# Kernel optimization log

Hardware: AMD Instinct MI355X
Metric: run time of the kernel (lower is better)

The kernel has to match this reference:

```python
import jax, jax.numpy as jnp
import numpy as np

B, T, W = 64, 64, 20
VIDEO_DIM = 1024
JOINT_DIM = 1024
K, STRIDE = 4, 4
MARGIN = 0.2
EPS = 1e-8


def _l2norm(x, axis=-1):
    n = jnp.sqrt(jnp.sum(x * x, axis=axis, keepdims=True))
    return x / jnp.maximum(n, EPS)


def _conv1d(x, w, b, stride):
    # x: (B, C, L), w: (O, I, K) -> (B, O, L_out), VALID padding (padding=0)
    y = jax.lax.conv_general_dilated(x, w, (stride,), 'VALID',
                                     dimension_numbers=('NCH', 'OIH', 'NCH'))
    return y + b[None, :, None]


def _diag_loss(scores, margin):
    # faithful port of diag(): row/column margin costs with zeroed diagonal
    b = scores.shape[0]
    d = jnp.diagonal(scores)
    off = 1.0 - jnp.eye(b, dtype=scores.dtype)
    cost_s = jnp.maximum(margin + scores - d[:, None], 0.0) * off
    cost_im = jnp.maximum(margin + scores - d[None, :], 0.0) * off
    return cost_s.sum() / b + cost_im.sum() / b


def setup_inputs() -> dict:
    key = jax.random.key(0)
    ks = jax.random.split(key, 10)
    def g(k, shape, scale=0.02):
        return jax.random.normal(k, shape, dtype=jnp.float32) * scale
    return dict(
        video=jax.random.normal(ks[0], (B, T, VIDEO_DIM), dtype=jnp.float32),
        words=jax.random.normal(ks[1], (B, W, JOINT_DIM), dtype=jnp.float32),
        w_masks=jnp.ones((B, W), dtype=jnp.int32),
        sentences=jax.random.normal(ks[2], (B, JOINT_DIM), dtype=jnp.float32),
        conv0_w=g(ks[3], (JOINT_DIM, VIDEO_DIM, K)),
        conv0_b=jnp.zeros((JOINT_DIM,), jnp.float32),
        conv1_w=g(ks[4], (JOINT_DIM, JOINT_DIM, K)),
        conv1_b=jnp.zeros((JOINT_DIM,), jnp.float32),
        conv2_w=g(ks[5], (JOINT_DIM, JOINT_DIM, K)),
        conv2_b=jnp.zeros((JOINT_DIM,), jnp.float32),
        conv1d_w=g(ks[6], (JOINT_DIM, JOINT_DIM, 1)),
        conv1d_b=jnp.zeros((JOINT_DIM,), jnp.float32),
        fc_w=g(ks[7], (JOINT_DIM, JOINT_DIM)),
        fc_b=jnp.zeros((JOINT_DIM,), jnp.float32),
    )


def reference(video, words, w_masks, sentences,
              conv0_w, conv0_b, conv1_w, conv1_b, conv2_w, conv2_b,
              conv1d_w, conv1d_b, fc_w, fc_b):
    # Vectorizes the original per-sample python loop over the pair axes (i=sentence, j=video).
    x = jnp.transpose(video, (0, 2, 1))          # (B, C, T)
    wmask = (w_masks > 0)                        # (B, W)
    conv_params = [(conv0_w, conv0_b), (conv1_w, conv1_b), (conv2_w, conv2_b)]
    sims = []
    v_tmp = x
    for cw, cb in conv_params:
        v_tmp = jax.nn.relu(_conv1d(v_tmp, cw, cb, STRIDE))
        v = jnp.transpose(_conv1d(v_tmp, conv1d_w, conv1d_b, 1), (0, 2, 1))  # (B, Tl, D)
        # frame_by_word: masked softmax attention of frames over words
        att = jnp.einsum('jtd,iwd->ijtw', v, words)            # (i, j, Tl, W)
        att = jnp.where(wmask[:, None, None, :], att, -1e30)
        att = jax.nn.softmax(att, axis=-1)
        v_s = jnp.einsum('ijtw,iwd->ijtd', att, words)         # attended word ctx
        # cosine sim of l2-normed vectors == dot product
        sim = jnp.einsum('jtd,ijtd->ijt', _l2norm(v), _l2norm(v_s))
        sims.append(sim)
    score_all = jnp.concatenate(sims, axis=2)    # (B, B, T_total=21)
    # torch code sorts descending then means over dim 1 -> mean is sort-invariant
    scores = score_all.mean(axis=2)              # (B, B) local scores
    positive_map = score_all[jnp.arange(B), jnp.arange(B)]     # (B, T_total)
    # global branch: final conv output has length 1 -> squeeze
    g_v = _l2norm(v_tmp[:, :, 0] @ fc_w.T + fc_b)              # (B, D), unit norm
    g_scores = _l2norm(sentences) @ g_v.T                      # [i, j] = cos(g_v[j], sent[i])
    loss = _diag_loss(scores, MARGIN) + _diag_loss(g_scores, MARGIN)
    return loss, positive_map
```

## Files before the change

kernel.cpp:

```cpp
#include <hip/hip_runtime.h>
#include <cmath>
#include <cstdint>


typedef __bf16 bf16_t;
typedef bf16_t bf16x8 __attribute__((ext_vector_type(8)));
typedef bf16_t bf16x4 __attribute__((ext_vector_type(4)));
typedef float  f32x4  __attribute__((ext_vector_type(4)));

__device__ __forceinline__ void gload_lds16(const void* g, void* l) {
    __builtin_amdgcn_global_load_lds(
        (const __attribute__((address_space(1))) void*)g,
        (__attribute__((address_space(3))) void*)l, 16, 0, 0);
}

__device__ __forceinline__ int swz(int r, int c) { return (r * 8 + (c ^ (r & 7))) * 8; }

__device__ __forceinline__ int remap1(int gm) {
    if (gm < 1024) return (gm >> 4) * 21 + (gm & 15);
    if (gm < 1280) { int g = gm - 1024; return (g >> 2) * 21 + 16 + (g & 3); }
    return (gm - 1280) * 21 + 20;
}

__global__ void prep_kernel(
    const float* __restrict__ c0w, const float* __restrict__ c1w,
    const float* __restrict__ c2w,
    bf16_t* __restrict__ WT0, bf16_t* __restrict__ WT1, bf16_t* __restrict__ WT2,
    const float* __restrict__ video, bf16_t* __restrict__ Vb,
    const float* __restrict__ words, bf16_t* __restrict__ Wordsb,
    const float* __restrict__ c1dw, bf16_t* __restrict__ C1b,
    const float* __restrict__ fcw, bf16_t* __restrict__ Fb)
{
    int bx = blockIdx.x;
    if (bx < 12288) {
        const float* w; bf16_t* wt;
        if (bx < 4096)      { w = c0w; wt = WT0; }
        else if (bx < 8192) { w = c1w; wt = WT1; bx -= 4096; }
        else                { w = c2w; wt = WT2; bx -= 8192; }
        int idx = bx * 256 + threadIdx.x;
        int i = idx & 1023, o = idx >> 10;
        float4 v = *(const float4*)(w + ((size_t)o << 12) + (i << 2));
        bf16_t* base = wt + ((size_t)o << 12) + i;
        base[0]    = (bf16_t)v.x;
        base[1024] = (bf16_t)v.y;
        base[2048] = (bf16_t)v.z;
        base[3072] = (bf16_t)v.w;
    } else {
        const float* s; bf16_t* d;
        if (bx < 16384)      { s = video; d = Vb;     bx -= 12288; }
        else if (bx < 17664) { s = words; d = Wordsb; bx -= 16384; }
        else if (bx < 18688) { s = c1dw;  d = C1b;    bx -= 17664; }
        else                 { s = fcw;   d = Fb;     bx -= 18688; }
        int off = (bx * 256 + threadIdx.x) * 4;
        float4 v = *(const float4*)(s + off);
        bf16x4 o4 = { (bf16_t)v.x, (bf16_t)v.y, (bf16_t)v.z, (bf16_t)v.w };
        *(bf16x4*)(d + off) = o4;
    }
}

__global__ __launch_bounds__(256) void mgemm_kernel(
    const bf16_t* __restrict__ A, const bf16_t* __restrict__ B,
    const bf16_t* __restrict__ B2, float* __restrict__ CP,
    int N, int K, int Kchunk, int fcTile, int aRow0, int cpSlice)
{
    __shared__ __align__(16) bf16_t sA[2][4096];
    __shared__ __align__(16) bf16_t sB[2][4096];
    const int tid  = threadIdx.x;
    const int lane = tid & 63;
    const int wave = tid >> 6;
    const int bx = blockIdx.x;
    const int m0C = bx * 64;
    int m0A = m0C;
    const bf16_t* Buse = B;
    if (bx == fcTile) { m0A = aRow0; Buse = B2; }
    const int n0 = blockIdx.y * 64;
    const int k0 = blockIdx.z * Kchunk;

    const int sr = tid >> 3;
    const int pc = tid & 7;
    const int lc = pc ^ (sr & 7);
    const bf16_t* Ag = A + (size_t)(m0A + sr) * K + lc * 8;
    const bf16_t* Bg = Buse + (size_t)(n0 + sr) * K + lc * 8;
    const size_t rowskip = (size_t)32 * K;

    const int wr = (wave >> 1) * 32;
    const int wc = (wave & 1) * 32;
    const int fm = lane & 15;
    const int cb = lane >> 4;

    int offA[2][2], offB[2][2];
    #pragma unroll
    for (int h = 0; h < 2; h++) {
        offA[h][0] = swz(wr +      fm, cb + h * 4);
        offA[h][1] = swz(wr + 16 + fm, cb + h * 4);
        offB[h][0] = swz(wc +      fm, cb + h * 4);
        offB[h][1] = swz(wc + 16 + fm, cb + h * 4);
    }

    f32x4 acc[2][2];
    #pragma unroll
    for (int a = 0; a < 2; a++)
        #pragma unroll
        for (int b = 0; b < 2; b++) acc[a][b] = (f32x4){0.f, 0.f, 0.f, 0.f};

    const int nIt = Kchunk >> 6;
    {
        const bf16_t* a = Ag + k0; const bf16_t* b = Bg + k0;
        gload_lds16(a,           &sA[0][tid * 8]);
        gload_lds16(a + rowskip, &sA[0][2048 + tid * 8]);
        gload_lds16(b,           &sB[0][tid * 8]);
        gload_lds16(b + rowskip, &sB[0][2048 + tid * 8]);
    }
    for (int it = 0; it < nIt; ++it) {
        const int buf = it & 1;
        __syncthreads();
        if (it + 1 < nIt) {
            const bf16_t* a = Ag + k0 + (it + 1) * 64;
            const bf16_t* b = Bg + k0 + (it + 1) * 64;
            bf16_t* dA = &sA[buf ^ 1][0];
            bf16_t* dB = &sB[buf ^ 1][0];
            gload_lds16(a,           dA + tid * 8);
            gload_lds16(a + rowskip, dA + 2048 + tid * 8);
            gload_lds16(b,           dB + tid * 8);
            gload_lds16(b + rowskip, dB + 2048 + tid * 8);
        }
        #pragma unroll
        for (int h = 0; h < 2; h++) {
            bf16x8 a0 = *(const bf16x8*)&sA[buf][offA[h][0]];
            bf16x8 a1 = *(const bf16x8*)&sA[buf][offA[h][1]];
            bf16x8 b0 = *(const bf16x8*)&sB[buf][offB[h][0]];
            bf16x8 b1 = *(const bf16x8*)&sB[buf][offB[h][1]];
            acc[0][0] = __builtin_amdgcn_mfma_f32_16x16x32_bf16(a0, b0, acc[0][0], 0, 0, 0);
            acc[0][1] = __builtin_amdgcn_mfma_f32_16x16x32_bf16(a0, b1, acc[0][1], 0, 0, 0);
            acc[1][0] = __builtin_amdgcn_mfma_f32_16x16x32_bf16(a1, b0, acc[1][0], 0, 0, 0);
            acc[1][1] = __builtin_amdgcn_mfma_f32_16x16x32_bf16(a1, b1, acc[1][1], 0, 0, 0);
        }
    }

    float* Cz = CP + (size_t)blockIdx.z * cpSlice;
    #pragma unroll
    for (int im = 0; im < 2; im++)
        #pragma unroll
        for (int rr = 0; rr < 4; rr++) {
            int gm = m0C + wr + im * 16 + (lane >> 4) * 4 + rr;
            #pragma unroll
            for (int in_ = 0; in_ < 2; in_++) {
                int cg = n0 + wc + in_ * 16 + (lane & 15);
                Cz[(size_t)gm * N + cg] = acc[im][in_][rr];
            }
        }
}

__global__ void epilogueB_kernel(const float* __restrict__ CP_, int nz,
    const float* __restrict__ bias, bf16_t* __restrict__ D, int MN, int N, int relu)
{
    int idx = blockIdx.x * 256 + threadIdx.x;
    if (idx >= MN) return;
    int n = idx % N;
    float s = 0.f;
    for (int z = 0; z < nz; z++) s += CP_[(size_t)z * MN + idx];
    if (bias) s += bias[n];
    if (relu) s = fmaxf(s, 0.f);
    D[idx] = (bf16_t)s;
}

__global__ void epilogueCF_kernel(const float* __restrict__ CP_,
    const float* __restrict__ bias1, const float* __restrict__ biasf,
    bf16_t* __restrict__ VCb, float* __restrict__ GV)
{
    int idx = blockIdx.x * 256 + threadIdx.x;
    int row = idx >> 10, n = idx & 1023;
    float s = CP_[idx] + CP_[idx + 1441792] + CP_[idx + 2 * 1441792] + CP_[idx + 3 * 1441792];
    if (row < 1344) VCb[(size_t)remap1(row) * 1024 + n] = (bf16_t)(s + bias1[n]);
    else            GV[(size_t)(row - 1344) * 1024 + n] = s + biasf[n];
}

__global__ void normgram_kernel(const bf16_t* __restrict__ VCb, float* __restrict__ VN,
                                const bf16_t* __restrict__ Wb, float* __restrict__ G)
{
    int bx = blockIdx.x;
    if (bx < 1344) {
        const bf16_t* x = VCb + ((size_t)bx << 10);
        float s = 0.f;
        for (int d = threadIdx.x; d < 1024; d += 256) { float v = (float)x[d]; s += v * v; }
        #pragma unroll
        for (int o = 32; o; o >>= 1) s += __shfl_xor(s, o, 64);
        __shared__ float red[4];
        if ((threadIdx.x & 63) == 0) red[threadIdx.x >> 6] = s;
        __syncthreads();
        if (threadIdx.x == 0) VN[bx] = sqrtf(red[0] + red[1] + red[2] + red[3]);
    } else {
        int g = bx - 1344;
        int i = g / 100, piece = g % 100;
        int wave = threadIdx.x >> 6, lane = threadIdx.x & 63;
        int pair = piece * 4 + wave;
        int w = pair / 20, w2 = pair % 20;
        const bf16_t* a = Wb + (((size_t)i * 20 + w)  << 10) + lane * 16;
        const bf16_t* b = Wb + (((size_t)i * 20 + w2) << 10) + lane * 16;
        bf16x8 a0 = *(const bf16x8*)a, a1 = *(const bf16x8*)(a + 8);
        bf16x8 b0 = *(const bf16x8*)b, b1 = *(const bf16x8*)(b + 8);
        float s = 0.f;
        #pragma unroll
        for (int e = 0; e < 8; e++)
            s += (float)a0[e] * (float)b0[e] + (float)a1[e] * (float)b1[e];
        #pragma unroll
        for (int o = 32; o; o >>= 1) s += __shfl_xor(s, o, 64);
        if (lane == 0) G[(size_t)i * 400 + pair] = s;
    }
}

__global__ __launch_bounds__(256) void sim_kernel(
    const float* __restrict__ CPat, const float* __restrict__ G_,
    const float* __restrict__ VN_, const int* __restrict__ wmask,
    float* __restrict__ SA_)
{
    __shared__ float Gs[400];
    __shared__ float msk[20];
    const int i  = blockIdx.x;
    const int jt = blockIdx.y * 256 + threadIdx.x;
    for (int q = threadIdx.x; q < 400; q += 256) Gs[q] = G_[(size_t)i * 400 + q];
    if (threadIdx.x < 20) msk[threadIdx.x] = (wmask[i * 20 + threadIdx.x] != 0) ? 1.f : 0.f;
    __syncthreads();
    if (jt >= 1344) return;

    float s[20], p[20];
    float mx = -1e30f;
    #pragma unroll
    for (int w = 0; w < 20; w++) {
        size_t q = (size_t)(i * 20 + w) * 1344 + jt;
        s[w] = CPat[q] + CPat[q + 1720320];
        if (msk[w] != 0.f) mx = fmaxf(mx, s[w]);
    }
    float denom = 0.f, num = 0.f;
    #pragma unroll
    for (int w = 0; w < 20; w++) {
        p[w] = (msk[w] != 0.f) ? __expf(s[w] - mx) : 0.f;
        denom += p[w];
        num   += p[w] * s[w];
    }
    float quad = 0.f;
    #pragma unroll
    for (int w = 0; w < 20; w++) {
        float c = 0.f;
        #pragma unroll
        for (int w2 = 0; w2 < 20; w2++) c += Gs[w * 20 + w2] * p[w2];
        quad += p[w] * c;
    }
    float dot = num / denom;
    float vsn = sqrtf(fmaxf(quad, 0.f)) / denom;
    float sim = dot / (fmaxf(VN_[jt], 1e-8f) * fmaxf(vsn, 1e-8f));
    SA_[(size_t)i * 1344 + jt] = sim;
}

__global__ void scores_l2_kernel(const float* __restrict__ SA_, float* __restrict__ SC_,
                                 float* __restrict__ out,
                                 const float* __restrict__ GV, float* __restrict__ GN,
                                 const float* __restrict__ sent, float* __restrict__ SN)
{
    int bx = blockIdx.x;
    if (bx < 16) {
        int idx = bx * 256 + threadIdx.x;
        int i = idx >> 6, j = idx & 63;
        const float* row = SA_ + (size_t)idx * 21;
        float s = 0.f;
        #pragma unroll
        for (int t = 0; t < 21; t++) s += row[t];
        SC_[idx] = s * (1.0f / 21.0f);
        if (i == j) {
            #pragma unroll
            for (int t = 0; t < 21; t++) out[1 + i * 21 + t] = row[t];
        }
    } else {
        int b2 = bx - 16;
        int r = b2 & 63;
        const float* x = (b2 < 64 ? GV : sent) + ((size_t)r << 10);
        float*       y = (b2 < 64 ? GN : SN)   + ((size_t)r << 10);
        float s = 0.f;
        for (int d = threadIdx.x; d < 1024; d += 256) { float v = x[d]; s += v * v; }
        #pragma unroll
        for (int o = 32; o; o >>= 1) s += __shfl_xor(s, o, 64);
        __shared__ float red[4];
        __shared__ float tot;
        if ((threadIdx.x & 63) == 0) red[threadIdx.x >> 6] = s;
        __syncthreads();
        if (threadIdx.x == 0) tot = 1.0f / fmaxf(sqrtf(red[0] + red[1] + red[2] + red[3]), 1e-8f);
        __syncthreads();
        float inv = tot;
        for (int d = threadIdx.x; d < 1024; d += 256) y[d] = x[d] * inv;
    }
}

__global__ void gscore_kernel(const float* __restrict__ SN_, const float* __restrict__ GN_,
                              float* __restrict__ GS_) {
    int item = blockIdx.x * 4 + (threadIdx.x >> 6);
    int i = item >> 6, j = item & 63;
    int lane = threadIdx.x & 63;
    const float* a = SN_ + (size_t)i * 1024;
    const float* b = GN_ + (size_t)j * 1024;
    float s = 0.f;
    #pragma unroll
    for (int q = 0; q < 16; q++) { int d = lane + 64 * q; s += a[d] * b[d]; }
    #pragma unroll
    for (int o = 32; o; o >>= 1) s += __shfl_xor(s, o, 64);
    if (lane == 0) GS_[item] = s;
}

__global__ void loss_kernel(const float* __restrict__ SC_, const float* __restrict__ GS_,
                            float* __restrict__ out) {
    __shared__ float d1[64], d2[64], red[4];
    int tid = threadIdx.x;
    if (tid < 64) { d1[tid] = SC_[tid * 65]; d2[tid] = GS_[tid * 65]; }
    __syncthreads();
    float acc = 0.f;
    for (int idx = tid; idx < 4096; idx += 256) {
        int i = idx >> 6, j = idx & 63;
        if (i != j) {
            float s = SC_[idx];
            acc += fmaxf(0.2f + s - d1[i], 0.f) + fmaxf(0.2f + s - d1[j], 0.f);
            float g = GS_[idx];
            acc += fmaxf(0.2f + g - d2[i], 0.f) + fmaxf(0.2f + g - d2[j], 0.f);
        }
    }
    #pragma unroll
    for (int o = 32; o; o >>= 1) acc += __shfl_xor(acc, o, 64);
    if ((tid & 63) == 0) red[tid >> 6] = acc;
    __syncthreads();
    if (tid == 0) out[0] = (red[0] + red[1] + red[2] + red[3]) * (1.0f / 64.0f);
}

extern "C" void kernel_launch(void* const* d_in, const int* in_sizes, int n_in,
                              void* d_out, int out_size, void* d_ws, size_t ws_size,
                              hipStream_t stream)
{
    const float* video     = (const float*)d_in[0];
    const float* words     = (const float*)d_in[1];
    const int*   w_masks   = (const int*)  d_in[2];
    const float* sentences = (const float*)d_in[3];
    const float* conv0_w   = (const float*)d_in[4];
    const float* conv0_b   = (const float*)d_in[5];
    const float* conv1_w   = (const float*)d_in[6];
    const float* conv1_b   = (const float*)d_in[7];
    const float* conv2_w   = (const float*)d_in[8];
    const float* conv2_b   = (const float*)d_in[9];
    const float* conv1d_w  = (const float*)d_in[10];
    const float* conv1d_b  = (const float*)d_in[11];
    const float* fc_w      = (const float*)d_in[12];
    const float* fc_b      = (const float*)d_in[13];
    float* out = (float*)d_out;
    float* ws = (float*)d_ws;

    bf16_t* WT0    = (bf16_t*)(ws + 0);
    bf16_t* WT1    = (bf16_t*)(ws + 2097152);
    bf16_t* WT2    = (bf16_t*)(ws + 4194304);
    bf16_t* Vb     = (bf16_t*)(ws + 6291456);
    bf16_t* Wordsb = (bf16_t*)(ws + 8388608);
    bf16_t* C1b    = (bf16_t*)(ws + 9043968);
    bf16_t* Fb     = (bf16_t*)(ws + 9568256);
    bf16_t* Astack = (bf16_t*)(ws + 10092544);
    bf16_t* VCb    = (bf16_t*)(ws + 10780672);
    float*  CP0    = ws + 11468800;
    float*  CP1    = ws + 15663104;
    float*  CP2    = ws + 19857408;
    float*  CPcf   = ws + 21954560;
    float*  CPat   = ws + 27721728;
    float*  VN     = ws + 31162368;
    float*  GR     = ws + 31163712;
    float*  SA     = ws + 31189312;
    float*  SC     = ws + 31275328;
    float*  GV     = ws + 31279424;
    float*  GN     = ws + 31344960;
    float*  SN     = ws + 31410496;
    float*  GS     = ws + 31476032;

    bf16_t* A2b = Astack + 1048576;
    bf16_t* A3b = Astack + 1310720;

    dim3 blk(256);

    prep_kernel<<<19712, blk, 0, stream>>>(
        conv0_w, conv1_w, conv2_w, WT0, WT1, WT2,
        video, Vb, words, Wordsb, conv1d_w, C1b, fc_w, Fb);

    mgemm_kernel<<<dim3(16,16,4), blk, 0, stream>>>(
        Vb, WT0, nullptr, CP0, 1024, 4096, 1024, -1, 0, 1048576);
    epilogueB_kernel<<<4096, blk, 0, stream>>>(CP0, 4, conv0_b, Astack, 1048576, 1024, 1);

    mgemm_kernel<<<dim3(4,16,16), blk, 0, stream>>>(
        Astack, WT1, nullptr, CP1, 1024, 4096, 256, -1, 0, 262144);
    epilogueB_kernel<<<1024, blk, 0, stream>>>(CP1, 16, conv1_b, A2b, 262144, 1024, 1);

    mgemm_kernel<<<dim3(1,16,32), blk, 0, stream>>>(
        A2b, WT2, nullptr, CP2, 1024, 4096, 128, -1, 0, 65536);
    epilogueB_kernel<<<256, blk, 0, stream>>>(CP2, 32, conv2_b, A3b, 65536, 1024, 1);

    mgemm_kernel<<<dim3(22,16,4), blk, 0, stream>>>(
        Astack, C1b, Fb, CPcf, 1024, 1024, 256, 21, 1280, 1441792);
    epilogueCF_kernel<<<5632, blk, 0, stream>>>(CPcf, conv1d_b, fc_b, VCb, GV);

    mgemm_kernel<<<dim3(20,21,2), blk, 0, stream>>>(
        Wordsb, VCb, nullptr, CPat, 1344, 1024, 512, -1, 0, 1720320);

    normgram_kernel<<<7744, blk, 0, stream>>>(VCb, VN, Wordsb, GR);
    sim_kernel<<<dim3(64,6), blk, 0, stream>>>(CPat, GR, VN, w_masks, SA);
    scores_l2_kernel<<<144, blk, 0, stream>>>(SA, SC, out, GV, GN, sentences, SN);
    gscore_kernel<<<1024, blk, 0, stream>>>(SN, GN, GS);
    loss_kernel<<<1, blk, 0, stream>>>(SC, GS, out);
}
```

Before: 242.8 us.

## Add 128x128-tile MFMA GEMM for conv0 and attention GEMMs

Adds a new GEMM kernel with 128x128 output tiles (4x4 MFMA fragments per wave, single-buffered LDS) and uses it for the first conv GEMM and the words-by-video attention GEMM. Larger tiles raise arithmetic intensity and cut redundant global loads compared with the 64x64 kernel. The conv0 split-K grows from 4 to 8 slices, which doubles the partial buffer and the epilogue reduction traffic. The attention output is padded to 1408 columns, so the workspace offsets and sim_kernel strides change with it. The new kernel drops double buffering, so loads are not overlapped with compute, and the padded VCb rows read beyond 1344 must stay in bounds.

```diff
diff --git a/kernel.cpp b/kernel.cpp
--- a/kernel.cpp
+++ b/kernel.cpp
@@ -58,6 +58,87 @@
     }
 }
 
+__global__ __launch_bounds__(256, 2) void mgemm128_kernel(
+    const bf16_t* __restrict__ A, const bf16_t* __restrict__ B,
+    float* __restrict__ CP, int N, int K, int Kchunk, int cpSlice)
+{
+    __shared__ __align__(16) bf16_t sA[8192];
+    __shared__ __align__(16) bf16_t sB[8192];
+    const int tid  = threadIdx.x;
+    const int lane = tid & 63;
+    const int wave = tid >> 6;
+    const int m0 = blockIdx.x * 128, n0 = blockIdx.y * 128;
+    const int k0 = blockIdx.z * Kchunk;
+
+    const int sr = tid >> 3;
+    const int pc = tid & 7;
+    const int lc = pc ^ (sr & 7);
+    const bf16_t* Ag = A + (size_t)(m0 + sr) * K + lc * 8 + k0;
+    const bf16_t* Bg = B + (size_t)(n0 + sr) * K + lc * 8 + k0;
+    const size_t rs = (size_t)32 * K;
+
+    const int wr = (wave >> 1) * 64;
+    const int wc = (wave & 1) * 64;
+    const int fm = lane & 15;
+    const int cb = lane >> 4;
+
+    int offA[2][4], offB[2][4];
+    #pragma unroll
+    for (int h = 0; h < 2; h++)
+        #pragma unroll
+        for (int f = 0; f < 4; f++) {
+            offA[h][f] = swz(wr + 16 * f + fm, cb + h * 4);
+            offB[h][f] = swz(wc + 16 * f + fm, cb + h * 4);
+        }
+
+    f32x4 acc[4][4];
+    #pragma unroll
+    for (int a = 0; a < 4; a++)
+        #pragma unroll
+        for (int b = 0; b < 4; b++) acc[a][b] = (f32x4){0.f, 0.f, 0.f, 0.f};
+
+    const int nIt = Kchunk >> 6;
+    for (int it = 0; it < nIt; ++it) {
+        __syncthreads();
+        const bf16_t* a = Ag + it * 64;
+        const bf16_t* b = Bg + it * 64;
+        #pragma unroll
+        for (int q = 0; q < 4; q++) {
+            gload_lds16(a + q * rs, sA + (tid + 256 * q) * 8);
+            gload_lds16(b + q * rs, sB + (tid + 256 * q) * 8);
+        }
+        __syncthreads();
+        #pragma unroll
+        for (int h = 0; h < 2; h++) {
+            bf16x8 av[4], bv[4];
+            #pragma unroll
+            for (int f = 0; f < 4; f++) {
+                av[f] = *(const bf16x8*)&sA[offA[h][f]];
+                bv[f] = *(const bf16x8*)&sB[offB[h][f]];
+            }
+            #pragma unroll
+            for (int ia = 0; ia < 4; ia++)
+                #pragma unroll
+                for (int ib = 0; ib < 4; ib++)
+                    acc[ia][ib] = __builtin_amdgcn_mfma_f32_16x16x32_bf16(
+                        av[ia], bv[ib], acc[ia][ib], 0, 0, 0);
+        }
+    }
+
+    float* Cz = CP + (size_t)blockIdx.z * cpSlice;
+    #pragma unroll
+    for (int ia = 0; ia < 4; ia++)
+        #pragma unroll
+        for (int rr = 0; rr < 4; rr++) {
+            int gm = m0 + wr + 16 * ia + cb * 4 + rr;
+            #pragma unroll
+            for (int ib = 0; ib < 4; ib++) {
+                int cg = n0 + wc + 16 * ib + fm;
+                Cz[(size_t)gm * N + cg] = acc[ia][ib][rr];
+            }
+        }
+}
+
 __global__ __launch_bounds__(256) void mgemm_kernel(
     const bf16_t* __restrict__ A, const bf16_t* __restrict__ B,
     const bf16_t* __restrict__ B2, float* __restrict__ CP,
@@ -142,10 +223,10 @@
     for (int im = 0; im < 2; im++)
         #pragma unroll
         for (int rr = 0; rr < 4; rr++) {
-            int gm = m0C + wr + im * 16 + (lane >> 4) * 4 + rr;
+            int gm = m0C + wr + im * 16 + cb * 4 + rr;
             #pragma unroll
             for (int in_ = 0; in_ < 2; in_++) {
-                int cg = n0 + wc + in_ * 16 + (lane & 15);
+                int cg = n0 + wc + in_ * 16 + fm;
                 Cz[(size_t)gm * N + cg] = acc[im][in_][rr];
             }
         }
@@ -227,8 +308,8 @@
     float mx = -1e30f;
     #pragma unroll
     for (int w = 0; w < 20; w++) {
-        size_t q = (size_t)(i * 20 + w) * 1344 + jt;
-        s[w] = CPat[q] + CPat[q + 1720320];
+        size_t q = (size_t)(i * 20 + w) * 1408 + jt;
+        s[w] = CPat[q] + CPat[q + 1802240];
         if (msk[w] != 0.f) mx = fmaxf(mx, s[w]);
     }
     float denom = 0.f, num = 0.f;
@@ -359,18 +440,18 @@
     bf16_t* Astack = (bf16_t*)(ws + 10092544);
     bf16_t* VCb    = (bf16_t*)(ws + 10780672);
     float*  CP0    = ws + 11468800;
-    float*  CP1    = ws + 15663104;
-    float*  CP2    = ws + 19857408;
-    float*  CPcf   = ws + 21954560;
-    float*  CPat   = ws + 27721728;
-    float*  VN     = ws + 31162368;
-    float*  GR     = ws + 31163712;
-    float*  SA     = ws + 31189312;
-    float*  SC     = ws + 31275328;
-    float*  GV     = ws + 31279424;
-    float*  GN     = ws + 31344960;
-    float*  SN     = ws + 31410496;
-    float*  GS     = ws + 31476032;
+    float*  CP1    = ws + 19857408;
+    float*  CP2    = ws + 24051712;
+    float*  CPcf   = ws + 26148864;
+    float*  CPat   = ws + 31916032;
+    float*  VN     = ws + 35520512;
+    float*  GR     = ws + 35521856;
+    float*  SA     = ws + 35547456;
+    float*  SC     = ws + 35633472;
+    float*  GV     = ws + 35637568;
+    float*  GN     = ws + 35703104;
+    float*  SN     = ws + 35768640;
+    float*  GS     = ws + 35834176;
 
     bf16_t* A2b = Astack + 1048576;
     bf16_t* A3b = Astack + 1310720;
@@ -381,9 +462,9 @@
         conv0_w, conv1_w, conv2_w, WT0, WT1, WT2,
         video, Vb, words, Wordsb, conv1d_w, C1b, fc_w, Fb);
 
-    mgemm_kernel<<<dim3(16,16,4), blk, 0, stream>>>(
-        Vb, WT0, nullptr, CP0, 1024, 4096, 1024, -1, 0, 1048576);
-    epilogueB_kernel<<<4096, blk, 0, stream>>>(CP0, 4, conv0_b, Astack, 1048576, 1024, 1);
+    mgemm128_kernel<<<dim3(8,8,8), blk, 0, stream>>>(
+        Vb, WT0, CP0, 1024, 4096, 512, 1048576);
+    epilogueB_kernel<<<4096, blk, 0, stream>>>(CP0, 8, conv0_b, Astack, 1048576, 1024, 1);
 
     mgemm_kernel<<<dim3(4,16,16), blk, 0, stream>>>(
         Astack, WT1, nullptr, CP1, 1024, 4096, 256, -1, 0, 262144);
@@ -397,8 +478,8 @@
         Astack, C1b, Fb, CPcf, 1024, 1024, 256, 21, 1280, 1441792);
     epilogueCF_kernel<<<5632, blk, 0, stream>>>(CPcf, conv1d_b, fc_b, VCb, GV);
 
-    mgemm_kernel<<<dim3(20,21,2), blk, 0, stream>>>(
-        Wordsb, VCb, nullptr, CPat, 1344, 1024, 512, -1, 0, 1720320);
+    mgemm128_kernel<<<dim3(10,11,2), blk, 0, stream>>>(
+        Wordsb, VCb, CPat, 1408, 1024, 512, 1802240);
 
     normgram_kernel<<<7744, blk, 0, stream>>>(VCb, VN, Wordsb, GR);
     sim_kernel<<<dim3(64,6), blk, 0, stream>>>(CPat, GR, VN, w_masks, SA);
```

Result: slower. 252.6 us (+4.0%).

## Fuse sim and score reduction; fold L2 norms into global score kernel

Applied to the files above, without the earlier changes.

The per-pair similarity kernel and the per-row score averaging are merged into one kernel with one block per sentence. Sims are kept in shared memory and averaged in place, so the SA buffer round trip and the scores_l2 launch go away. The separate L2-normalize pass for global video and sentence vectors is dropped: gscore now computes both norms alongside the dot product. The cost is that the sim stage runs on only 64 blocks looping over 1344 columns instead of 384 blocks, which lowers parallelism on a wide GPU.

```diff
diff --git a/kernel.cpp b/kernel.cpp
--- a/kernel.cpp
+++ b/kernel.cpp
@@ -142,10 +142,10 @@
     for (int im = 0; im < 2; im++)
         #pragma unroll
         for (int rr = 0; rr < 4; rr++) {
-            int gm = m0C + wr + im * 16 + (lane >> 4) * 4 + rr;
+            int gm = m0C + wr + im * 16 + cb * 4 + rr;
             #pragma unroll
             for (int in_ = 0; in_ < 2; in_++) {
-                int cg = n0 + wc + in_ * 16 + (lane & 15);
+                int cg = n0 + wc + in_ * 16 + fm;
                 Cz[(size_t)gm * N + cg] = acc[im][in_][rr];
             }
         }
@@ -209,100 +209,84 @@
     }
 }
 
-__global__ __launch_bounds__(256) void sim_kernel(
+__global__ __launch_bounds__(256) void simscores_kernel(
     const float* __restrict__ CPat, const float* __restrict__ G_,
     const float* __restrict__ VN_, const int* __restrict__ wmask,
-    float* __restrict__ SA_)
+    float* __restrict__ SC_, float* __restrict__ out)
 {
     __shared__ float Gs[400];
     __shared__ float msk[20];
-    const int i  = blockIdx.x;
-    const int jt = blockIdx.y * 256 + threadIdx.x;
+    __shared__ float simbuf[1344];
+    const int i = blockIdx.x;
     for (int q = threadIdx.x; q < 400; q += 256) Gs[q] = G_[(size_t)i * 400 + q];
     if (threadIdx.x < 20) msk[threadIdx.x] = (wmask[i * 20 + threadIdx.x] != 0) ? 1.f : 0.f;
     __syncthreads();
-    if (jt >= 1344) return;
-
-    float s[20], p[20];
-    float mx = -1e30f;
-    #pragma unroll
-    for (int w = 0; w < 20; w++) {
-        size_t q = (size_t)(i * 20 + w) * 1344 + jt;
-        s[w] = CPat[q] + CPat[q + 1720320];
-        if (msk[w] != 0.f) mx = fmaxf(mx, s[w]);
-    }
-    float denom = 0.f, num = 0.f;
-    #pragma unroll
-    for (int w = 0; w < 20; w++) {
-        p[w] = (msk[w] != 0.f) ? __expf(s[w] - mx) : 0.f;
-        denom += p[w];
-        num   += p[w] * s[w];
-    }
-    float quad = 0.f;
-    #pragma unroll
-    for (int w = 0; w < 20; w++) {
-        float c = 0.f;
-        #pragma unroll
-        for (int w2 = 0; w2 < 20; w2++) c += Gs[w * 20 + w2] * p[w2];
-        quad += p[w] * c;
-    }
-    float dot = num / denom;
-    float vsn = sqrtf(fmaxf(quad, 0.f)) / denom;
-    float sim = dot / (fmaxf(VN_[jt], 1e-8f) * fmaxf(vsn, 1e-8f));
-    SA_[(size_t)i * 1344 + jt] = sim;
-}
-
-__global__ void scores_l2_kernel(const float* __restrict__ SA_, float* __restrict__ SC_,
-                                 float* __restrict__ out,
-                                 const float* __restrict__ GV, float* __restrict__ GN,
-                                 const float* __restrict__ sent, float* __restrict__ SN)
-{
-    int bx = blockIdx.x;
-    if (bx < 16) {
-        int idx = bx * 256 + threadIdx.x;
-        int i = idx >> 6, j = idx & 63;
-        const float* row = SA_ + (size_t)idx * 21;
+
+    for (int base = 0; base < 1344; base += 256) {
+        int jt = base + threadIdx.x;
+        if (jt < 1344) {
+            float s[20], p[20];
+            float mx = -1e30f;
+            #pragma unroll
+            for (int w = 0; w < 20; w++) {
+                size_t q = (size_t)(i * 20 + w) * 1344 + jt;
+                s[w] = CPat[q] + CPat[q + 1720320];
+                if (msk[w] != 0.f) mx = fmaxf(mx, s[w]);
+            }
+            float denom = 0.f, num = 0.f;
+            #pragma unroll
+            for (int w = 0; w < 20; w++) {
+                p[w] = (msk[w] != 0.f) ? __expf(s[w] - mx) : 0.f;
+                denom += p[w];
+                num   += p[w] * s[w];
+            }
+            float quad = 0.f;
+            #pragma unroll
+            for (int w = 0; w < 20; w++) {
+                float c = 0.f;
+                #pragma unroll
+                for (int w2 = 0; w2 < 20; w2++) c += Gs[w * 20 + w2] * p[w2];
+                quad += p[w] * c;
+            }
+            float dot = num / denom;
+            float vsn = sqrtf(fmaxf(quad, 0.f)) / denom;
+            float sim = dot / (fmaxf(VN_[jt], 1e-8f) * fmaxf(vsn, 1e-8f));
+            simbuf[jt] = sim;
+            if (jt / 21 == i) out[1 + i * 21 + (jt % 21)] = sim;
+        }
+    }
+    __syncthreads();
+    if (threadIdx.x < 64) {
+        int j = threadIdx.x;
         float s = 0.f;
         #pragma unroll
-        for (int t = 0; t < 21; t++) s += row[t];
-        SC_[idx] = s * (1.0f / 21.0f);
-        if (i == j) {
-            #pragma unroll
-            for (int t = 0; t < 21; t++) out[1 + i * 21 + t] = row[t];
-        }
-    } else {
-        int b2 = bx - 16;
-        int r = b2 & 63;
-        const float* x = (b2 < 64 ? GV : sent) + ((size_t)r << 10);
-        float*       y = (b2 < 64 ? GN : SN)   + ((size_t)r << 10);
-        float s = 0.f;
-        for (int d = threadIdx.x; d < 1024; d += 256) { float v = x[d]; s += v * v; }
-        #pragma unroll
-        for (int o = 32; o; o >>= 1) s += __shfl_xor(s, o, 64);
-        __shared__ float red[4];
-        __shared__ float tot;
-        if ((threadIdx.x & 63) == 0) red[threadIdx.x >> 6] = s;
-        __syncthreads();
-        if (threadIdx.x == 0) tot = 1.0f / fmaxf(sqrtf(red[0] + red[1] + red[2] + red[3]), 1e-8f);
-        __syncthreads();
-        float inv = tot;
-        for (int d = threadIdx.x; d < 1024; d += 256) y[d] = x[d] * inv;
-    }
-}
-
-__global__ void gscore_kernel(const float* __restrict__ SN_, const float* __restrict__ GN_,
+        for (int t = 0; t < 21; t++) s += simbuf[j * 21 + t];
+        SC_[i * 64 + j] = s * (1.0f / 21.0f);
+    }
+}
+
+__global__ void gscore_kernel(const float* __restrict__ sent, const float* __restrict__ GV,
                               float* __restrict__ GS_) {
     int item = blockIdx.x * 4 + (threadIdx.x >> 6);
     int i = item >> 6, j = item & 63;
     int lane = threadIdx.x & 63;
-    const float* a = SN_ + (size_t)i * 1024;
-    const float* b = GN_ + (size_t)j * 1024;
-    float s = 0.f;
-    #pragma unroll
-    for (int q = 0; q < 16; q++) { int d = lane + 64 * q; s += a[d] * b[d]; }
-    #pragma unroll
-    for (int o = 32; o; o >>= 1) s += __shfl_xor(s, o, 64);
-    if (lane == 0) GS_[item] = s;
+    const float* a = sent + (size_t)i * 1024;
+    const float* b = GV + (size_t)j * 1024;
+    float sab = 0.f, saa = 0.f, sbb = 0.f;
+    #pragma unroll
+    for (int q = 0; q < 16; q++) {
+        int d = lane + 64 * q;
+        float av = a[d], bv = b[d];
+        sab += av * bv; saa += av * av; sbb += bv * bv;
+    }
+    #pragma unroll
+    for (int o = 32; o; o >>= 1) {
+        sab += __shfl_xor(sab, o, 64);
+        saa += __shfl_xor(saa, o, 64);
+        sbb += __shfl_xor(sbb, o, 64);
+    }
+    if (lane == 0)
+        GS_[item] = sab / (fmaxf(sqrtf(saa), 1e-8f) * fmaxf(sqrtf(sbb), 1e-8f));
 }
 
 __global__ void loss_kernel(const float* __restrict__ SC_, const float* __restrict__ GS_,
@@ -365,12 +349,9 @@
     float*  CPat   = ws + 27721728;
     float*  VN     = ws + 31162368;
     float*  GR     = ws + 31163712;
-    float*  SA     = ws + 31189312;
-    float*  SC     = ws + 31275328;
-    float*  GV     = ws + 31279424;
-    float*  GN     = ws + 31344960;
-    float*  SN     = ws + 31410496;
-    float*  GS     = ws + 31476032;
+    float*  SC     = ws + 31189312;
+    float*  GV     = ws + 31193408;
+    float*  GS     = ws + 31258944;
 
     bf16_t* A2b = Astack + 1048576;
     bf16_t* A3b = Astack + 1310720;
@@ -401,8 +382,7 @@
         Wordsb, VCb, nullptr, CPat, 1344, 1024, 512, -1, 0, 1720320);
 
     normgram_kernel<<<7744, blk, 0, stream>>>(VCb, VN, Wordsb, GR);
-    sim_kernel<<<dim3(64,6), blk, 0, stream>>>(CPat, GR, VN, w_masks, SA);
-    scores_l2_kernel<<<144, blk, 0, stream>>>(SA, SC, out, GV, GN, sentences, SN);
-    gscore_kernel<<<1024, blk, 0, stream>>>(SN, GN, GS);
+    simscores_kernel<<<64, blk, 0, stream>>>(CPat, GR, VN, w_masks, SC, out);
+    gscore_kernel<<<1024, blk, 0, stream>>>(sentences, GV, GS);
     loss_kernel<<<1, blk, 0, stream>>>(SC, GS, out);
 }
```

After: 253.7 us. +4.5%, slower.
